# Kernel tuning notes

Measured on AMD Instinct MI355X. Metric: run time of the kernel, lower is better.

Reference implementation:

```python
import jax, jax.numpy as jnp
import numpy as np

N_FOOD = 50000
N_NUT = 50000
E = 800000
D = 128      # embedding_dim == hidden_dim
H = 4        # heads
C = D // H   # per-head channels
L = 2        # num_layers
NEG_SLOPE = 0.2


def _gat_conv(x_src, x_dst, ei, Wsrc, Wdst, a_src, a_dst, bias, n_dst):
    """PyG GATConv (bipartite, no self loops, concat heads, no edge_dim)."""
    hs = (x_src @ Wsrc).reshape(-1, H, C)   # [Ns, H, C]
    hd = (x_dst @ Wdst).reshape(-1, H, C)   # [Nd, H, C]
    src, dst = ei[0], ei[1]
    alpha_s = jnp.einsum('nhc,hc->nh', hs, a_src)  # [Ns, H]
    alpha_d = jnp.einsum('nhc,hc->nh', hd, a_dst)  # [Nd, H]
    e = alpha_s[src] + alpha_d[dst]                # [E, H]
    e = jax.nn.leaky_relu(e, NEG_SLOPE)
    # segment softmax over edges grouped by destination node
    emax = jax.ops.segment_max(e, dst, num_segments=n_dst)
    emax = jnp.where(jnp.isfinite(emax), emax, 0.0)
    ex = jnp.exp(e - emax[dst])
    denom = jax.ops.segment_sum(ex, dst, num_segments=n_dst)
    alpha = ex / (denom[dst] + 1e-16)              # [E, H]
    msg = hs[src] * alpha[:, :, None]              # [E, H, C]
    out = jax.ops.segment_sum(msg, dst, num_segments=n_dst)
    return out.reshape(n_dst, H * C) + bias


def setup_inputs() -> dict:
    key = jax.random.key(0)
    ks = jax.random.split(key, 16)
    w = 1.0 / np.sqrt(D)
    a = 1.0 / np.sqrt(C)
    inp = {
        'x_food': jax.random.normal(ks[0], (N_FOOD, D), jnp.float32),
        'x_nut': jax.random.normal(ks[1], (N_NUT, D), jnp.float32),
        'Wsrc_fn': jax.random.normal(ks[2], (L, D, D), jnp.float32) * w,
        'Wdst_fn': jax.random.normal(ks[3], (L, D, D), jnp.float32) * w,
        'att_src_fn': jax.random.normal(ks[4], (L, H, C), jnp.float32) * a,
        'att_dst_fn': jax.random.normal(ks[5], (L, H, C), jnp.float32) * a,
        'bias_fn': jnp.zeros((L, D), jnp.float32),
        'Wsrc_nf': jax.random.normal(ks[6], (L, D, D), jnp.float32) * w,
        'Wdst_nf': jax.random.normal(ks[7], (L, D, D), jnp.float32) * w,
        'att_src_nf': jax.random.normal(ks[8], (L, H, C), jnp.float32) * a,
        'att_dst_nf': jax.random.normal(ks[9], (L, H, C), jnp.float32) * a,
        'bias_nf': jnp.zeros((L, D), jnp.float32),
        'ei_fn': jax.random.randint(ks[10], (2, E), 0, N_FOOD, jnp.int32),  # food -> nutrient
        'ei_nf': jax.random.randint(ks[11], (2, E), 0, N_NUT, jnp.int32),   # nutrient -> food
    }
    return inp


def reference(x_food, x_nut, Wsrc_fn, Wdst_fn, att_src_fn, att_dst_fn, bias_fn,
              Wsrc_nf, Wdst_nf, att_src_nf, att_dst_nf, bias_nf, ei_fn, ei_nf):
    h_food, h_nut = x_food, x_nut
    for l in range(L):
        # relation food --contains--> nutrient (dst = nutrient)
        out_nut = _gat_conv(h_food, h_nut, ei_fn, Wsrc_fn[l], Wdst_fn[l],
                            att_src_fn[l], att_dst_fn[l], bias_fn[l], N_NUT)
        # relation nutrient --contained_in--> food (dst = food)
        out_food = _gat_conv(h_nut, h_food, ei_nf, Wsrc_nf[l], Wdst_nf[l],
                             att_src_nf[l], att_dst_nf[l], bias_nf[l], N_FOOD)
        # dropout is identity at inference; ELU activation
        h_food = jax.nn.elu(out_food)
        h_nut = jax.nn.elu(out_nut)
    return jnp.stack([h_food, h_nut])  # [2, 50000, 128]
```

## Files before the change

### kernel.cpp

```cpp
#include <hip/hip_runtime.h>
#include <math.h>

#define NNODE 50000
#define NEDGE 800000
#define DIM   128
#define NHEAD 4
#define NTILE ((NNODE + 63) / 64)
#define NBUCK 196
#define ECHUNK 196
#define CAP   6144

typedef __bf16 bf16x8 __attribute__((ext_vector_type(8)));
typedef float  f32x4  __attribute__((ext_vector_type(4)));
typedef float  f32x2  __attribute__((ext_vector_type(2)));

static __device__ __forceinline__ void bfsplit(float x, ushort& hi, ushort& lo) {
    __bf16 h = (__bf16)x;
    float hf = (float)h;
    __bf16 l = (__bf16)(x - hf);
    hi = __builtin_bit_cast(unsigned short, h);
    lo = __builtin_bit_cast(unsigned short, l);
}
static __device__ __forceinline__ ushort f2h(float x) {
    _Float16 h = (_Float16)x;
    return __builtin_bit_cast(unsigned short, h);
}
static __device__ __forceinline__ f32x2 up2v(unsigned u) {
    f32x2 r;
    r.x = (float)__builtin_bit_cast(_Float16, (unsigned short)(u & 0xffff));
    r.y = (float)__builtin_bit_cast(_Float16, (unsigned short)(u >> 16));
    return r;
}
static __device__ __forceinline__ unsigned encf(float f) {
    unsigned u = __builtin_bit_cast(unsigned, f);
    return (u >> 31) ? ~u : (u | 0x80000000u);
}
static __device__ __forceinline__ float decf(unsigned x) {
    unsigned u = (x >> 31) ? (x & 0x7fffffffu) : ~x;
    return __builtin_bit_cast(float, u);
}

__global__ __launch_bounds__(256) void bhist(const int* __restrict__ eA,
                                             const int* __restrict__ eB,
                                             int* __restrict__ bcnt) {
    int rel = (int)(blockIdx.x >= ECHUNK);
    const int* dstrow = (rel ? eB : eA) + NEDGE;
    int blk = blockIdx.x - rel * ECHUNK;
    __shared__ int hist[256];
    hist[threadIdx.x] = 0;
    __syncthreads();
    int base = blk * 4096;
    #pragma unroll
    for (int k = 0; k < 16; k++) {
        int e = base + k * 256 + threadIdx.x;
        if (e < NEDGE) atomicAdd(&hist[dstrow[e] >> 8], 1);
    }
    __syncthreads();
    int h = hist[threadIdx.x];
    if (h) atomicAdd(&bcnt[rel * 256 + threadIdx.x], h);
}

__global__ __launch_bounds__(256) void bscan(const int* __restrict__ bcnt,
                                             int* __restrict__ bko, int* __restrict__ bcur,
                                             int* __restrict__ ptrA, int* __restrict__ ptrB) {
    int rel = blockIdx.x;
    __shared__ int tmp[256];
    int t = threadIdx.x;
    int v = bcnt[rel * 256 + t];
    tmp[t] = v; __syncthreads();
    for (int off = 1; off < 256; off <<= 1) {
        int a = (t >= off) ? tmp[t - off] : 0; __syncthreads();
        tmp[t] += a; __syncthreads();
    }
    int excl = tmp[t] - v;
    bko[rel * 256 + t] = excl;
    bcur[rel * 256 + t] = excl;
    if (t == 255) (rel ? ptrB : ptrA)[NNODE] = tmp[255];
}

__global__ __launch_bounds__(256) void bscatter(const int* __restrict__ eA,
                                                const int* __restrict__ eB,
                                                int* __restrict__ bcur,
                                                unsigned* __restrict__ bktA,
                                                unsigned* __restrict__ bktB) {
    int rel = (int)(blockIdx.x >= ECHUNK);
    const int* ebase = rel ? eB : eA;
    unsigned* bkt = rel ? bktB : bktA;
    int blk = blockIdx.x - rel * ECHUNK;
    __shared__ int hist[256], bas[256], cur[256];
    hist[threadIdx.x] = 0;
    __syncthreads();
    int base = blk * 4096;
    #pragma unroll
    for (int k = 0; k < 16; k++) {
        int e = base + k * 256 + threadIdx.x;
        if (e < NEDGE) atomicAdd(&hist[ebase[NEDGE + e] >> 8], 1);
    }
    __syncthreads();
    int h = hist[threadIdx.x];
    bas[threadIdx.x] = h ? atomicAdd(&bcur[rel * 256 + threadIdx.x], h) : 0;
    cur[threadIdx.x] = 0;
    __syncthreads();
    #pragma unroll
    for (int k = 0; k < 16; k++) {
        int e = base + k * 256 + threadIdx.x;
        if (e < NEDGE) {
            int s = ebase[e], d = ebase[NEDGE + e];
            int b = d >> 8;
            int loc = atomicAdd(&cur[b], 1);
            bkt[bas[b] + loc] = ((unsigned)(d & 255) << 16) | (unsigned)s;
        }
    }
}

__global__ __launch_bounds__(256) void bsort(const unsigned* __restrict__ bktA,
                                             const unsigned* __restrict__ bktB,
                                             const int* __restrict__ bko,
                                             int* __restrict__ ptrA, int* __restrict__ ptrB,
                                             ushort* __restrict__ srcA, ushort* __restrict__ srcB) {
    int rel = (int)(blockIdx.x >= NBUCK);
    const unsigned* bkt = rel ? bktB : bktA;
    int* ptr   = rel ? ptrB : ptrA;
    ushort* srcs = rel ? srcB : srcA;
    int b = blockIdx.x - rel * NBUCK;
    int beg = bko[rel * 256 + b], end = bko[rel * 256 + b + 1];
    int cnt_e = end - beg;
    __shared__ int hist[256], excl[256], cur[256];
    __shared__ unsigned sorted[CAP];
    int t = threadIdx.x;
    hist[t] = 0;
    __syncthreads();
    for (int i = t; i < cnt_e; i += 256) atomicAdd(&hist[bkt[beg + i] >> 16], 1);
    __syncthreads();
    int v = hist[t];
    excl[t] = v; __syncthreads();
    for (int off = 1; off < 256; off <<= 1) {
        int a = (t >= off) ? excl[t - off] : 0; __syncthreads();
        excl[t] += a; __syncthreads();
    }
    int ex = excl[t] - v;
    int d = b * 256 + t;
    if (d < NNODE) ptr[d] = beg + ex;
    cur[t] = ex;
    __syncthreads();
    for (int i = t; i < cnt_e; i += 256) {
        unsigned u = bkt[beg + i];
        int dl = u >> 16;
        int p = atomicAdd(&cur[dl], 1);
        if (p < CAP) sorted[p] = u;
        else srcs[beg + p] = (ushort)(u & 0xffffu);
    }
    __syncthreads();
    int lim = cnt_e < CAP ? cnt_e : CAP;
    for (int i = t; i < lim; i += 256) {
        unsigned u = sorted[i];
        srcs[beg + i] = (ushort)(u & 0xffffu);
    }
}

__global__ void prep_wav(const float* __restrict__ Wsrc_fn, const float* __restrict__ a_src_fn,
                         const float* __restrict__ Wdst_fn, const float* __restrict__ a_dst_fn,
                         const float* __restrict__ Wsrc_nf, const float* __restrict__ a_src_nf,
                         const float* __restrict__ Wdst_nf, const float* __restrict__ a_dst_nf,
                         float* __restrict__ wav) {
    int call = blockIdx.x;
    int layer = call >> 1, which = call & 1;
    const float* Ws = which ? Wsrc_nf : Wsrc_fn;
    const float* as = which ? a_src_nf : a_src_fn;
    const float* Wd = which ? Wdst_fn : Wdst_nf;
    const float* ad = which ? a_dst_fn : a_dst_nf;
    Ws += layer * DIM * DIM; Wd += layer * DIM * DIM;
    as += layer * DIM; ad += layer * DIM;
    for (int it = threadIdx.x; it < 512; it += 256) {
        int k = it >> 2, h = it & 3;
        float s = 0.f, dv = 0.f;
        #pragma unroll 8
        for (int c = 0; c < 32; c++) {
            s  += Ws[k * DIM + h * 32 + c] * as[h * 32 + c];
            dv += Wd[k * DIM + h * 32 + c] * ad[h * 32 + c];
        }
        float* o = wav + (size_t)call * DIM * 8 + k * 8;
        o[h] = s; o[h + 4] = dv;
    }
}

__global__ __launch_bounds__(256, 3) void transform_kernel(
    const float* __restrict__ XA, const float* __restrict__ WA, const float* __restrict__ wavA,
    ushort* __restrict__ HSA, float* __restrict__ ASA, float* __restrict__ ADA,
    const float* __restrict__ XB, const float* __restrict__ WB, const float* __restrict__ wavB,
    ushort* __restrict__ HSB, float* __restrict__ ASB, float* __restrict__ ADB,
    unsigned* __restrict__ Mg, int nb)
{
    int rel = (int)(blockIdx.x >= (unsigned)nb);
    const float* X  = rel ? XB : XA;
    const float* W  = rel ? WB : WA;
    const float* wav = rel ? wavB : wavA;
    ushort* HS = rel ? HSB : HSA;
    float*  AS = rel ? ASB : ASA;
    float*  AD = rel ? ADB : ADA;

    __shared__ ushort WTh[64][136], WTl[64][136];
    __shared__ ushort wavTh[16][136], wavTl[16][136];
    __shared__ unsigned mloc[4];

    int vb = blockIdx.x - rel * nb;
    int half = vb & 1;
    int ch = half * 64;

    for (int i = threadIdx.x; i < 64 * DIM; i += 256) {
        int col = i & 63, k = i >> 6;
        ushort hi, lo; bfsplit(W[k * DIM + ch + col], hi, lo);
        WTh[col][k] = hi; WTl[col][k] = lo;
    }
    for (int i = threadIdx.x; i < 16 * DIM; i += 256) {
        int c = i & 15, k = i >> 4;
        float w = (c < 8) ? wav[k * 8 + c] : 0.f;
        ushort hi, lo; bfsplit(w, hi, lo);
        wavTh[c][k] = hi; wavTl[c][k] = lo;
    }
    if (threadIdx.x < 4) mloc[threadIdx.x] = 0;
    __syncthreads();

    const int wv = threadIdx.x >> 6, lane = threadIdx.x & 63;
    const int lm = lane & 15, lq = lane >> 4;
    const int r0 = wv * 16;

    for (int tile = vb >> 1; tile < NTILE; tile += (nb >> 1)) {
        int row0 = tile * 64;
        int myrow = row0 + r0 + lm;
        int rowc = myrow < NNODE ? myrow : NNODE - 1;
        const float4* Xr = (const float4*)(X + (size_t)rowc * DIM);

        float4 xv[8];
        #pragma unroll
        for (int kc = 0; kc < 4; kc++) {
            xv[kc * 2]     = Xr[kc * 8 + lq * 2];
            xv[kc * 2 + 1] = Xr[kc * 8 + lq * 2 + 1];
        }

        f32x4 acc[4] = {{0,0,0,0},{0,0,0,0},{0,0,0,0},{0,0,0,0}};
        f32x4 accv = {0,0,0,0};
        #pragma unroll
        for (int kc = 0; kc < 4; kc++) {
            const float* fp = (const float*)&xv[kc * 2];
            bf16x8 ah, al;
            #pragma unroll
            for (int j = 0; j < 8; j++) {
                float x = fp[j];
                __bf16 h = (__bf16)x;
                ah[j] = h;
                al[j] = (__bf16)(x - (float)h);
            }
            int k0 = kc * 32 + lq * 8;
            #pragma unroll
            for (int ct = 0; ct < 4; ct++) {
                bf16x8 bh = *(const bf16x8*)&WTh[ct * 16 + lm][k0];
                bf16x8 bl = *(const bf16x8*)&WTl[ct * 16 + lm][k0];
                acc[ct] = __builtin_amdgcn_mfma_f32_16x16x32_bf16(al, bh, acc[ct], 0, 0, 0);
                acc[ct] = __builtin_amdgcn_mfma_f32_16x16x32_bf16(ah, bl, acc[ct], 0, 0, 0);
                acc[ct] = __builtin_amdgcn_mfma_f32_16x16x32_bf16(ah, bh, acc[ct], 0, 0, 0);
            }
            if (half == 0) {
                bf16x8 vh = *(const bf16x8*)&wavTh[lm][k0];
                bf16x8 vl = *(const bf16x8*)&wavTl[lm][k0];
                accv = __builtin_amdgcn_mfma_f32_16x16x32_bf16(al, vh, accv, 0, 0, 0);
                accv = __builtin_amdgcn_mfma_f32_16x16x32_bf16(ah, vl, accv, 0, 0, 0);
                accv = __builtin_amdgcn_mfma_f32_16x16x32_bf16(ah, vh, accv, 0, 0, 0);
            }
        }

        #pragma unroll
        for (int ct = 0; ct < 4; ct++) {
            #pragma unroll
            for (int r = 0; r < 4; r++) {
                int row = row0 + r0 + lq * 4 + r;
                if (row < NNODE) HS[(size_t)row * DIM + ch + ct * 16 + lm] = f2h(acc[ct][r]);
            }
        }
        if (half == 0 && lm < 8) {
            float mx4 = -INFINITY;
            #pragma unroll
            for (int r = 0; r < 4; r++) {
                int row = row0 + r0 + lq * 4 + r;
                if (row < NNODE) {
                    if (lm < 4) AS[row * 4 + lm] = accv[r];
                    else        AD[row * 4 + (lm - 4)] = accv[r];
                }
                mx4 = fmaxf(mx4, accv[r]);
            }
            if (lm < 4) atomicMax(&mloc[lm], encf(mx4));
        }
    }
    __syncthreads();
    if (half == 0 && threadIdx.x < 4)
        atomicMax(&Mg[rel * 4 + threadIdx.x], mloc[threadIdx.x]);
}

__global__ __launch_bounds__(256) void agg_kernel(
    const ushort* __restrict__ HSA, const float* __restrict__ ASA, const float* __restrict__ ADA,
    const int* __restrict__ ptrA, const ushort* __restrict__ srcA,
    const float* __restrict__ biasA, float* __restrict__ outA,
    const ushort* __restrict__ HSB, const float* __restrict__ ASB, const float* __restrict__ ADB,
    const int* __restrict__ ptrB, const ushort* __restrict__ srcB,
    const float* __restrict__ biasB, float* __restrict__ outB,
    const unsigned* __restrict__ Mg, int nb)
{
    int rel = (int)(blockIdx.x >= (unsigned)nb);
    const unsigned* HSu = (const unsigned*)(rel ? HSB : HSA);
    const float* AS = rel ? ASB : ASA;
    const float* AD = rel ? ADB : ADA;
    const ushort* srcs = rel ? srcB : srcA;
    const int* ptr = rel ? ptrB : ptrA;
    const float* bias = rel ? biasB : biasA;
    float* out = rel ? outB : outA;

    int bid = blockIdx.x - rel * nb;
    int wave = threadIdx.x >> 6, lane = threadIdx.x & 63;
    int d = bid * 4 + wave;
    if (d >= NNODE) return;
    int hh = lane >> 4;

    float ad_h = AD[d * 4 + hh];
    float mm = decf(Mg[rel * 4 + hh]) + ad_h;
    mm = mm > 0.f ? mm : 0.2f * mm;

    int e0 = ptr[d], e1 = ptr[d + 1];

    f32x2 acc0 = {0.f, 0.f}, acc1 = acc0, acc2 = acc0, acc3 = acc0;
    float l0 = 0.f, l1 = 0.f, l2 = 0.f, l3 = 0.f;
    int e = e0;

    for (; e + 8 <= e1; e += 8) {
        ushort sv[8];
        #pragma unroll
        for (int k = 0; k < 8; k++) sv[k] = srcs[e + k];
        unsigned u[8]; float av[8];
        #pragma unroll
        for (int k = 0; k < 8; k++) {
            int s = __builtin_amdgcn_readfirstlane((int)sv[k]);
            u[k] = HSu[(s << 6) + lane];
            av[k] = AS[(s << 2) + hh];
        }
        #pragma unroll
        for (int k = 0; k < 8; k++) {
            float v = av[k] + ad_h;
            v = v > 0.f ? v : 0.2f * v;
            float p = __expf(v - mm);
            f32x2 h = up2v(u[k]);
            if ((k & 3) == 0)      { acc0 += h * p; l0 += p; }
            else if ((k & 3) == 1) { acc1 += h * p; l1 += p; }
            else if ((k & 3) == 2) { acc2 += h * p; l2 += p; }
            else                   { acc3 += h * p; l3 += p; }
        }
    }
    for (; e + 4 <= e1; e += 4) {
        ushort sv[4];
        #pragma unroll
        for (int k = 0; k < 4; k++) sv[k] = srcs[e + k];
        unsigned u[4]; float av[4];
        #pragma unroll
        for (int k = 0; k < 4; k++) {
            int s = __builtin_amdgcn_readfirstlane((int)sv[k]);
            u[k] = HSu[(s << 6) + lane];
            av[k] = AS[(s << 2) + hh];
        }
        #pragma unroll
        for (int k = 0; k < 4; k++) {
            float v = av[k] + ad_h;
            v = v > 0.f ? v : 0.2f * v;
            float p = __expf(v - mm);
            f32x2 h = up2v(u[k]);
            if (k == 0)      { acc0 += h * p; l0 += p; }
            else if (k == 1) { acc1 += h * p; l1 += p; }
            else if (k == 2) { acc2 += h * p; l2 += p; }
            else             { acc3 += h * p; l3 += p; }
        }
    }
    for (; e < e1; e++) {
        int s = __builtin_amdgcn_readfirstlane((int)srcs[e]);
        unsigned u = HSu[(s << 6) + lane];
        float v = AS[(s << 2) + hh] + ad_h;
        v = v > 0.f ? v : 0.2f * v;
        float p = __expf(v - mm);
        f32x2 h = up2v(u);
        acc0 += h * p; l0 += p;
    }

    f32x2 acc = (acc0 + acc1) + (acc2 + acc3);
    float l = (l0 + l1) + (l2 + l3);

    int j0 = lane * 2;
    float inv = 1.f / (l + 1e-16f);
    float o0 = acc.x * inv + bias[j0];
    float o1 = acc.y * inv + bias[j0 + 1];
    o0 = o0 > 0.f ? o0 : __expf(o0) - 1.f;
    o1 = o1 > 0.f ? o1 : __expf(o1) - 1.f;
    *(float2*)&out[(size_t)d * DIM + j0] = make_float2(o0, o1);
}

extern "C" void kernel_launch(void* const* d_in, const int* in_sizes, int n_in,
                              void* d_out, int out_size, void* d_ws, size_t ws_size,
                              hipStream_t stream) {
    const float* x_food      = (const float*)d_in[0];
    const float* x_nut       = (const float*)d_in[1];
    const float* Wsrc_fn     = (const float*)d_in[2];
    const float* Wdst_fn     = (const float*)d_in[3];
    const float* att_src_fn  = (const float*)d_in[4];
    const float* att_dst_fn  = (const float*)d_in[5];
    const float* bias_fn     = (const float*)d_in[6];
    const float* Wsrc_nf     = (const float*)d_in[7];
    const float* Wdst_nf     = (const float*)d_in[8];
    const float* att_src_nf  = (const float*)d_in[9];
    const float* att_dst_nf  = (const float*)d_in[10];
    const float* bias_nf     = (const float*)d_in[11];
    const int*   ei_fn       = (const int*)d_in[12];
    const int*   ei_nf       = (const int*)d_in[13];
    float* out = (float*)d_out;

    char* ws = (char*)d_ws;
    size_t off = 0;
    auto alloc_f = [&](size_t n) { float* p = (float*)(ws + off); off += n * 4; return p; };
    auto alloc_i = [&](size_t n) { int* p = (int*)(ws + off); off += n * 4; return p; };
    auto alloc_u = [&](size_t n) { ushort* p = (ushort*)(ws + off); off += n * 2; return p; };

    float* B_food = alloc_f((size_t)NNODE * DIM);
    float* B_nut  = alloc_f((size_t)NNODE * DIM);
    ushort* HS_fn = alloc_u((size_t)NNODE * DIM);
    ushort* HS_nf = alloc_u((size_t)NNODE * DIM);
    float* AS_fn  = alloc_f(NNODE * NHEAD);
    float* AS_nf  = alloc_f(NNODE * NHEAD);
    float* AD_fn  = alloc_f(NNODE * NHEAD);
    float* AD_nf  = alloc_f(NNODE * NHEAD);
    float* wav    = alloc_f(4 * DIM * 8);
    int* ptr_fn   = alloc_i(50004);
    int* ptr_nf   = alloc_i(50004);
    ushort* srcs_fn = alloc_u(NEDGE);
    ushort* srcs_nf = alloc_u(NEDGE);
    int* bcnt     = alloc_i(512);
    unsigned* Mbuf = (unsigned*)alloc_i(16);
    int* bko      = alloc_i(512);
    int* bcur     = alloc_i(512);
    unsigned* bkt_fn = (unsigned*)B_food;
    unsigned* bkt_nf = (unsigned*)B_nut;

    hipMemsetAsync(bcnt, 0, (512 + 16) * 4, stream);
    bhist<<<2 * ECHUNK, 256, 0, stream>>>(ei_fn, ei_nf, bcnt);
    bscan<<<2, 256, 0, stream>>>(bcnt, bko, bcur, ptr_fn, ptr_nf);
    bscatter<<<2 * ECHUNK, 256, 0, stream>>>(ei_fn, ei_nf, bcur, bkt_fn, bkt_nf);
    bsort<<<2 * NBUCK, 256, 0, stream>>>(bkt_fn, bkt_nf, bko, ptr_fn, ptr_nf,
                                         srcs_fn, srcs_nf);

    prep_wav<<<4, 256, 0, stream>>>(Wsrc_fn, att_src_fn, Wdst_fn, att_dst_fn,
                                    Wsrc_nf, att_src_nf, Wdst_nf, att_dst_nf, wav);

    const int WL = DIM * DIM;
    const int TNB = 768;
    const int ANB = (NNODE + 3) / 4;
    float* wav0 = wav;
    float* wav1 = wav + DIM * 8;
    float* wav2 = wav + 2 * DIM * 8;
    float* wav3 = wav + 3 * DIM * 8;

    transform_kernel<<<2 * TNB, 256, 0, stream>>>(
        x_food, Wsrc_fn, wav0, HS_fn, AS_fn, AD_nf,
        x_nut,  Wsrc_nf, wav1, HS_nf, AS_nf, AD_fn, Mbuf, TNB);
    agg_kernel<<<2 * ANB, 256, 0, stream>>>(
        HS_fn, AS_fn, AD_fn, ptr_fn, srcs_fn, bias_fn, B_nut,
        HS_nf, AS_nf, AD_nf, ptr_nf, srcs_nf, bias_nf, B_food, Mbuf, ANB);

    transform_kernel<<<2 * TNB, 256, 0, stream>>>(
        B_food, Wsrc_fn + WL, wav2, HS_fn, AS_fn, AD_nf,
        B_nut,  Wsrc_nf + WL, wav3, HS_nf, AS_nf, AD_fn, Mbuf + 8, TNB);
    agg_kernel<<<2 * ANB, 256, 0, stream>>>(
        HS_fn, AS_fn, AD_fn, ptr_fn, srcs_fn, bias_fn + DIM, out + (size_t)NNODE * DIM,
        HS_nf, AS_nf, AD_nf, ptr_nf, srcs_nf, bias_nf + DIM, out, Mbuf + 8, ANB);
}
```

Baseline: 437.8 us.

## Split wave into four edge groups with 16-byte row gathers in aggregation

The aggregation kernel now has each quarter-wave handle a different edge, with each lane loading 16 bytes (8 fp16 channels) of the source row instead of 4 bytes. The four partial sums are combined with cross-lane shuffles before the output is written. Attention logits are pre-scaled by log2(e) in the projection kernel so the softmax can use the native exp2 instruction. This raises memory-level parallelism for the gather and uses wider loads, at the cost of shuffle reductions and having only one quarter of the wave do the final store.

```diff
diff --git a/kernel.cpp b/kernel.cpp
--- a/kernel.cpp
+++ b/kernel.cpp
@@ -9,6 +9,7 @@
 #define NBUCK 196
 #define ECHUNK 196
 #define CAP   6144
+#define LOG2E 1.44269504088896340736f
 
 typedef __bf16 bf16x8 __attribute__((ext_vector_type(8)));
 typedef float  f32x4  __attribute__((ext_vector_type(4)));
@@ -278,6 +279,7 @@
             }
         }
         if (half == 0 && lm < 8) {
+            accv *= LOG2E;
             float mx4 = -INFINITY;
             #pragma unroll
             for (int r = 0; r < 4; r++) {
@@ -306,7 +308,7 @@
     const unsigned* __restrict__ Mg, int nb)
 {
     int rel = (int)(blockIdx.x >= (unsigned)nb);
-    const unsigned* HSu = (const unsigned*)(rel ? HSB : HSA);
+    const uint4* HS4 = (const uint4*)(rel ? HSB : HSA);
     const float* AS = rel ? ASB : ASA;
     const float* AD = rel ? ADB : ADA;
     const ushort* srcs = rel ? srcB : srcA;
@@ -318,7 +320,10 @@
     int wave = threadIdx.x >> 6, lane = threadIdx.x & 63;
     int d = bid * 4 + wave;
     if (d >= NNODE) return;
-    int hh = lane >> 4;
+
+    int q  = lane >> 4;
+    int li = lane & 15;
+    int hh = li >> 2;
 
     float ad_h = AD[d * 4 + hh];
     float mm = decf(Mg[rel * 4 + hh]) + ad_h;
@@ -326,76 +331,73 @@
 
     int e0 = ptr[d], e1 = ptr[d + 1];
 
-    f32x2 acc0 = {0.f, 0.f}, acc1 = acc0, acc2 = acc0, acc3 = acc0;
-    float l0 = 0.f, l1 = 0.f, l2 = 0.f, l3 = 0.f;
+    float acc[8] = {0.f,0.f,0.f,0.f,0.f,0.f,0.f,0.f};
+    float l = 0.f;
+
     int e = e0;
-
     for (; e + 8 <= e1; e += 8) {
-        ushort sv[8];
-        #pragma unroll
-        for (int k = 0; k < 8; k++) sv[k] = srcs[e + k];
-        unsigned u[8]; float av[8];
-        #pragma unroll
-        for (int k = 0; k < 8; k++) {
-            int s = __builtin_amdgcn_readfirstlane((int)sv[k]);
-            u[k] = HSu[(s << 6) + lane];
-            av[k] = AS[(s << 2) + hh];
-        }
-        #pragma unroll
-        for (int k = 0; k < 8; k++) {
-            float v = av[k] + ad_h;
-            v = v > 0.f ? v : 0.2f * v;
-            float p = __expf(v - mm);
-            f32x2 h = up2v(u[k]);
-            if ((k & 3) == 0)      { acc0 += h * p; l0 += p; }
-            else if ((k & 3) == 1) { acc1 += h * p; l1 += p; }
-            else if ((k & 3) == 2) { acc2 += h * p; l2 += p; }
-            else                   { acc3 += h * p; l3 += p; }
-        }
-    }
-    for (; e + 4 <= e1; e += 4) {
-        ushort sv[4];
-        #pragma unroll
-        for (int k = 0; k < 4; k++) sv[k] = srcs[e + k];
-        unsigned u[4]; float av[4];
-        #pragma unroll
-        for (int k = 0; k < 4; k++) {
-            int s = __builtin_amdgcn_readfirstlane((int)sv[k]);
-            u[k] = HSu[(s << 6) + lane];
-            av[k] = AS[(s << 2) + hh];
-        }
-        #pragma unroll
-        for (int k = 0; k < 4; k++) {
-            float v = av[k] + ad_h;
-            v = v > 0.f ? v : 0.2f * v;
-            float p = __expf(v - mm);
-            f32x2 h = up2v(u[k]);
-            if (k == 0)      { acc0 += h * p; l0 += p; }
-            else if (k == 1) { acc1 += h * p; l1 += p; }
-            else if (k == 2) { acc2 += h * p; l2 += p; }
-            else             { acc3 += h * p; l3 += p; }
-        }
-    }
-    for (; e < e1; e++) {
-        int s = __builtin_amdgcn_readfirstlane((int)srcs[e]);
-        unsigned u = HSu[(s << 6) + lane];
-        float v = AS[(s << 2) + hh] + ad_h;
-        v = v > 0.f ? v : 0.2f * v;
-        float p = __expf(v - mm);
-        f32x2 h = up2v(u);
-        acc0 += h * p; l0 += p;
-    }
-
-    f32x2 acc = (acc0 + acc1) + (acc2 + acc3);
-    float l = (l0 + l1) + (l2 + l3);
-
-    int j0 = lane * 2;
-    float inv = 1.f / (l + 1e-16f);
-    float o0 = acc.x * inv + bias[j0];
-    float o1 = acc.y * inv + bias[j0 + 1];
-    o0 = o0 > 0.f ? o0 : __expf(o0) - 1.f;
-    o1 = o1 > 0.f ? o1 : __expf(o1) - 1.f;
-    *(float2*)&out[(size_t)d * DIM + j0] = make_float2(o0, o1);
+        int iA = e + q, iB = e + 4 + q;
+        int sA = srcs[iA], sB = srcs[iB];
+        uint4 hA = HS4[sA * 16 + li];
+        uint4 hB = HS4[sB * 16 + li];
+        float aA = AS[sA * 4 + hh];
+        float aB = AS[sB * 4 + hh];
+        float vA = aA + ad_h; vA = fmaxf(vA, 0.2f * vA);
+        float vB = aB + ad_h; vB = fmaxf(vB, 0.2f * vB);
+        float pA = __builtin_amdgcn_exp2f(vA - mm);
+        float pB = __builtin_amdgcn_exp2f(vB - mm);
+        l += pA + pB;
+        #pragma unroll
+        for (int j = 0; j < 4; j++) {
+            f32x2 h2A = up2v(((const unsigned*)&hA)[j]);
+            f32x2 h2B = up2v(((const unsigned*)&hB)[j]);
+            acc[2*j]   += h2A.x * pA + h2B.x * pB;
+            acc[2*j+1] += h2A.y * pA + h2B.y * pB;
+        }
+    }
+    for (; e < e1; e += 4) {
+        int ee = e + q;
+        bool act = ee < e1;
+        int eidx = act ? ee : e1 - 1;
+        int s = srcs[eidx];
+        uint4 hv = HS4[s * 16 + li];
+        float av = AS[s * 4 + hh];
+        float v = av + ad_h; v = fmaxf(v, 0.2f * v);
+        float p = __builtin_amdgcn_exp2f(v - mm);
+        p = act ? p : 0.f;
+        l += p;
+        #pragma unroll
+        for (int j = 0; j < 4; j++) {
+            f32x2 h2 = up2v(((const unsigned*)&hv)[j]);
+            acc[2*j]   += h2.x * p;
+            acc[2*j+1] += h2.y * p;
+        }
+    }
+
+    #pragma unroll
+    for (int j = 0; j < 8; j++) {
+        acc[j] += __shfl_xor(acc[j], 16, 64);
+        acc[j] += __shfl_xor(acc[j], 32, 64);
+    }
+    l += __shfl_xor(l, 16, 64);
+    l += __shfl_xor(l, 32, 64);
+
+    if (q == 0) {
+        float inv = 1.f / (l + 1e-16f);
+        const float4* b4 = (const float4*)bias + li * 2;
+        float4 b0 = b4[0], b1 = b4[1];
+        float o[8];
+        o[0] = acc[0] * inv + b0.x; o[1] = acc[1] * inv + b0.y;
+        o[2] = acc[2] * inv + b0.z; o[3] = acc[3] * inv + b0.w;
+        o[4] = acc[4] * inv + b1.x; o[5] = acc[5] * inv + b1.y;
+        o[6] = acc[6] * inv + b1.z; o[7] = acc[7] * inv + b1.w;
+        #pragma unroll
+        for (int j = 0; j < 8; j++)
+            o[j] = o[j] > 0.f ? o[j] : __expf(o[j]) - 1.f;
+        float4* o4 = (float4*)(out + (size_t)d * DIM) + li * 2;
+        o4[0] = make_float4(o[0], o[1], o[2], o[3]);
+        o4[1] = make_float4(o[4], o[5], o[6], o[7]);
+    }
 }
 
 extern "C" void kernel_launch(void* const* d_in, const int* in_sizes, int n_in,
```

Result: faster. 423.5 us (-3.3%).
